# Kernel optimization log

Hardware: AMD Instinct MI355X
Metric: run time of the kernel (lower is better)

The kernel has to match this reference:

```python
import jax, jax.numpy as jnp
import numpy as np

NUM_GLOBAL_EXPERTS = 256
LOCAL_START = 64  # global experts [64, 128) live on this rank


def setup_inputs() -> dict:
    key = jax.random.key(0)
    k1, = jax.random.split(key, 1)
    num_local_experts = 64
    # Routing ids: ~4.2M tokens x topk=8, values are GLOBAL expert ids in [0, 256)
    topk_ids = jax.random.randint(k1, (33554432,), 0, NUM_GLOBAL_EXPERTS, dtype=jnp.int32)
    # expert_map: global -> local; -1 for experts not owned by this rank
    gid = jnp.arange(NUM_GLOBAL_EXPERTS, dtype=jnp.int32)
    expert_map = jnp.where(
        (gid >= LOCAL_START) & (gid < LOCAL_START + num_local_experts),
        gid - LOCAL_START,
        jnp.int32(-1),
    )
    return {"topk_ids": topk_ids, "num_local_experts": num_local_experts, "expert_map": expert_map}


def reference(topk_ids, num_local_experts, expert_map=None):
    n = num_local_experts  # static python int
    ids = topk_ids.reshape(-1)
    if expert_map is not None:
        # invalid ids (< 0) stay invalid; valid global ids are remapped to local space
        ids = jnp.where(ids >= 0, expert_map[jnp.clip(ids, 0)], jnp.int32(-1))
    # Route all invalid / out-of-range ids into an overflow bucket n, then drop it.
    valid = (ids >= 0) & (ids < n)
    bucket = jnp.where(valid, ids, jnp.int32(n))
    counts = jax.ops.segment_sum(
        jnp.ones_like(bucket, dtype=jnp.int32), bucket, num_segments=n + 1
    )
    return counts[:n].astype(jnp.int32)
```

## Files before the change

kernel.cpp:

```cpp
#include <hip/hip_runtime.h>

#define BLOCK   256
#define NB1     2048
#define NBINS   256
#define NWAVES  (BLOCK / 64)
#define UNROLL  4

__global__ __launch_bounds__(BLOCK) void hist_part(const int* __restrict__ ids,
                                                   int N,
                                                   int* __restrict__ partials) {
    __shared__ int lds[NWAVES * NBINS];
    const int tid = threadIdx.x;
    for (int i = tid; i < NWAVES * NBINS; i += BLOCK) lds[i] = 0;
    __syncthreads();

    int* h = &lds[(tid >> 6) * NBINS];

    const int4* __restrict__ ids4 = (const int4*)ids;
    const int n4      = N >> 2;
    const int chunk   = BLOCK * UNROLL;
    const int gstride = (int)gridDim.x * chunk;
    const int n4_full = (n4 / gstride) * gstride;

    for (int i = (int)blockIdx.x * chunk + tid; i < n4_full; i += gstride) {
        int4 v[UNROLL];
#pragma unroll
        for (int u = 0; u < UNROLL; ++u) v[u] = ids4[i + u * BLOCK];
#pragma unroll
        for (int u = 0; u < UNROLL; ++u) {
            atomicAdd(&h[v[u].x & (NBINS - 1)], 1);
            atomicAdd(&h[v[u].y & (NBINS - 1)], 1);
            atomicAdd(&h[v[u].z & (NBINS - 1)], 1);
            atomicAdd(&h[v[u].w & (NBINS - 1)], 1);
        }
    }
    for (int i = n4_full + (int)blockIdx.x * BLOCK + tid; i < n4;
         i += (int)gridDim.x * BLOCK) {
        int4 v = ids4[i];
        atomicAdd(&h[v.x & (NBINS - 1)], 1);
        atomicAdd(&h[v.y & (NBINS - 1)], 1);
        atomicAdd(&h[v.z & (NBINS - 1)], 1);
        atomicAdd(&h[v.w & (NBINS - 1)], 1);
    }
    if (blockIdx.x == 0) {
        for (int i = (n4 << 2) + tid; i < N; i += BLOCK)
            atomicAdd(&h[ids[i] & (NBINS - 1)], 1);
    }
    __syncthreads();

    for (int b = tid; b < NBINS; b += BLOCK) {
        int s = 0;
#pragma unroll
        for (int w = 0; w < NWAVES; ++w) s += lds[w * NBINS + b];
        partials[b * NB1 + blockIdx.x] = s;
    }
}

__global__ __launch_bounds__(BLOCK) void reduce_part(const int* __restrict__ partials,
                                                     const int* __restrict__ emap,
                                                     int emap_n,
                                                     int* __restrict__ out,
                                                     int n_local) {
    const int g = blockIdx.x;
    const int tid = threadIdx.x;
    int s = 0;
    for (int j = tid; j < NB1; j += BLOCK) s += partials[g * NB1 + j];
#pragma unroll
    for (int off = 32; off > 0; off >>= 1) s += __shfl_down(s, off, 64);
    __shared__ int wsum[NWAVES];
    if ((tid & 63) == 0) wsum[tid >> 6] = s;
    __syncthreads();
    if (tid == 0) {
        int tot = 0;
#pragma unroll
        for (int w = 0; w < NWAVES; ++w) tot += wsum[w];
        int l = (g < emap_n) ? emap[g] : -1;
        if ((unsigned)l < (unsigned)n_local && tot != 0) atomicAdd(&out[l], tot);
    }
}

extern "C" void kernel_launch(void* const* d_in, const int* in_sizes, int n_in,
                              void* d_out, int out_size, void* d_ws, size_t ws_size,
                              hipStream_t stream) {
    const int* topk_ids   = (const int*)d_in[0];
    const int* expert_map = (const int*)d_in[2];
    const int N       = in_sizes[0];
    const int emap_n  = in_sizes[2];
    const int n_local = out_size;

    int* partials = (int*)d_ws;

    hipMemsetAsync(d_out, 0, (size_t)n_local * sizeof(int), stream);

    hist_part<<<NB1, BLOCK, 0, stream>>>(topk_ids, N, partials);
    reduce_part<<<NBINS, BLOCK, 0, stream>>>(partials, expert_map, emap_n,
                                             (int*)d_out, n_local);
}
```

Baseline: 199.9 us.

## Remap expert ids inside histogram and skip non-local ids via affine map detection

Adds a prep kernel that checks whether expert_map is a contiguous affine range and records its base and count. The histogram kernel then either subtracts the base and bounds-checks, or looks each id up in an LDS copy of the map, so only local experts get atomics. This replaces the memset and the per-bin emap lookups in the reduce stage, and the reduce now runs over n_local bins only. The cost is an extra tiny kernel launch plus per-element compare and branch work, in exchange for roughly three quarters fewer LDS atomics.

```diff
diff --git a/kernel.cpp b/kernel.cpp
--- a/kernel.cpp
+++ b/kernel.cpp
@@ -6,15 +6,50 @@
 #define NWAVES  (BLOCK / 64)
 #define UNROLL  4
 
+#define PARTIALS_OFF 4096
+
+__global__ __launch_bounds__(BLOCK) void prep(const int* __restrict__ emap,
+                                              int emap_n,
+                                              int* __restrict__ params) {
+    __shared__ int s_min, s_cnt, s_ok;
+    const int tid = threadIdx.x;
+    if (tid == 0) { s_min = 0x7FFFFFFF; s_cnt = 0; s_ok = 1; }
+    __syncthreads();
+    for (int g = tid; g < emap_n; g += BLOCK) {
+        if (emap[g] >= 0) { atomicMin(&s_min, g); atomicAdd(&s_cnt, 1); }
+    }
+    __syncthreads();
+    const int lo = s_min, cnt = s_cnt;
+    for (int g = tid; g < emap_n; g += BLOCK) {
+        int expect = (g >= lo && g < lo + cnt) ? (g - lo) : -1;
+        if (emap[g] != expect) atomicAnd(&s_ok, 0);
+    }
+    __syncthreads();
+    if (tid == 0) { params[0] = lo; params[1] = cnt; params[2] = s_ok; }
+}
+
 __global__ __launch_bounds__(BLOCK) void hist_part(const int* __restrict__ ids,
                                                    int N,
-                                                   int* __restrict__ partials) {
-    __shared__ int lds[NWAVES * NBINS];
+                                                   const int* __restrict__ params,
+                                                   const int* __restrict__ emap,
+                                                   int emap_n,
+                                                   int* __restrict__ partials,
+                                                   int n_local) {
+    __shared__ int hist[NWAVES * NBINS];
+    __shared__ int lmap[NBINS];
     const int tid = threadIdx.x;
-    for (int i = tid; i < NWAVES * NBINS; i += BLOCK) lds[i] = 0;
+    const int lo = params[0];
+    const unsigned cnt = (unsigned)params[1];
+    const int affine = params[2];
+
+    for (int i = tid; i < NWAVES * NBINS; i += BLOCK) hist[i] = 0;
+    if (!affine) {
+        for (int i = tid; i < NBINS; i += BLOCK)
+            lmap[i] = (i < emap_n) ? emap[i] : -1;
+    }
     __syncthreads();
 
-    int* h = &lds[(tid >> 6) * NBINS];
+    int* h = &hist[(tid >> 6) * NBINS];
 
     const int4* __restrict__ ids4 = (const int4*)ids;
     const int n4      = N >> 2;
@@ -22,49 +57,92 @@
     const int gstride = (int)gridDim.x * chunk;
     const int n4_full = (n4 / gstride) * gstride;
 
-    for (int i = (int)blockIdx.x * chunk + tid; i < n4_full; i += gstride) {
-        int4 v[UNROLL];
+    if (affine) {
+        for (int i = (int)blockIdx.x * chunk + tid; i < n4_full; i += gstride) {
+            int4 v[UNROLL];
 #pragma unroll
-        for (int u = 0; u < UNROLL; ++u) v[u] = ids4[i + u * BLOCK];
+            for (int u = 0; u < UNROLL; ++u) v[u] = ids4[i + u * BLOCK];
 #pragma unroll
-        for (int u = 0; u < UNROLL; ++u) {
-            atomicAdd(&h[v[u].x & (NBINS - 1)], 1);
-            atomicAdd(&h[v[u].y & (NBINS - 1)], 1);
-            atomicAdd(&h[v[u].z & (NBINS - 1)], 1);
-            atomicAdd(&h[v[u].w & (NBINS - 1)], 1);
+            for (int u = 0; u < UNROLL; ++u) {
+                unsigned a = (unsigned)(v[u].x - lo);
+                unsigned b = (unsigned)(v[u].y - lo);
+                unsigned c = (unsigned)(v[u].z - lo);
+                unsigned d = (unsigned)(v[u].w - lo);
+                if (a < cnt) atomicAdd(&h[a], 1);
+                if (b < cnt) atomicAdd(&h[b], 1);
+                if (c < cnt) atomicAdd(&h[c], 1);
+                if (d < cnt) atomicAdd(&h[d], 1);
+            }
         }
-    }
-    for (int i = n4_full + (int)blockIdx.x * BLOCK + tid; i < n4;
-         i += (int)gridDim.x * BLOCK) {
-        int4 v = ids4[i];
-        atomicAdd(&h[v.x & (NBINS - 1)], 1);
-        atomicAdd(&h[v.y & (NBINS - 1)], 1);
-        atomicAdd(&h[v.z & (NBINS - 1)], 1);
-        atomicAdd(&h[v.w & (NBINS - 1)], 1);
-    }
-    if (blockIdx.x == 0) {
-        for (int i = (n4 << 2) + tid; i < N; i += BLOCK)
-            atomicAdd(&h[ids[i] & (NBINS - 1)], 1);
+        for (int i = n4_full + (int)blockIdx.x * BLOCK + tid; i < n4;
+             i += (int)gridDim.x * BLOCK) {
+            int4 v = ids4[i];
+            unsigned a = (unsigned)(v.x - lo), b = (unsigned)(v.y - lo);
+            unsigned c = (unsigned)(v.z - lo), d = (unsigned)(v.w - lo);
+            if (a < cnt) atomicAdd(&h[a], 1);
+            if (b < cnt) atomicAdd(&h[b], 1);
+            if (c < cnt) atomicAdd(&h[c], 1);
+            if (d < cnt) atomicAdd(&h[d], 1);
+        }
+        if (blockIdx.x == 0) {
+            for (int i = (n4 << 2) + tid; i < N; i += BLOCK) {
+                unsigned a = (unsigned)(ids[i] - lo);
+                if (a < cnt) atomicAdd(&h[a], 1);
+            }
+        }
+    } else {
+        for (int i = (int)blockIdx.x * chunk + tid; i < n4_full; i += gstride) {
+            int4 v[UNROLL];
+#pragma unroll
+            for (int u = 0; u < UNROLL; ++u) v[u] = ids4[i + u * BLOCK];
+#pragma unroll
+            for (int u = 0; u < UNROLL; ++u) {
+                int l0 = ((unsigned)v[u].x < NBINS) ? lmap[v[u].x] : -1;
+                int l1 = ((unsigned)v[u].y < NBINS) ? lmap[v[u].y] : -1;
+                int l2 = ((unsigned)v[u].z < NBINS) ? lmap[v[u].z] : -1;
+                int l3 = ((unsigned)v[u].w < NBINS) ? lmap[v[u].w] : -1;
+                if (l0 >= 0) atomicAdd(&h[l0], 1);
+                if (l1 >= 0) atomicAdd(&h[l1], 1);
+                if (l2 >= 0) atomicAdd(&h[l2], 1);
+                if (l3 >= 0) atomicAdd(&h[l3], 1);
+            }
+        }
+        for (int i = n4_full + (int)blockIdx.x * BLOCK + tid; i < n4;
+             i += (int)gridDim.x * BLOCK) {
+            int4 v = ids4[i];
+            int l0 = ((unsigned)v.x < NBINS) ? lmap[v.x] : -1;
+            int l1 = ((unsigned)v.y < NBINS) ? lmap[v.y] : -1;
+            int l2 = ((unsigned)v.z < NBINS) ? lmap[v.z] : -1;
+            int l3 = ((unsigned)v.w < NBINS) ? lmap[v.w] : -1;
+            if (l0 >= 0) atomicAdd(&h[l0], 1);
+            if (l1 >= 0) atomicAdd(&h[l1], 1);
+            if (l2 >= 0) atomicAdd(&h[l2], 1);
+            if (l3 >= 0) atomicAdd(&h[l3], 1);
+        }
+        if (blockIdx.x == 0) {
+            for (int i = (n4 << 2) + tid; i < N; i += BLOCK) {
+                int v = ids[i];
+                int l = ((unsigned)v < NBINS) ? lmap[v] : -1;
+                if (l >= 0) atomicAdd(&h[l], 1);
+            }
+        }
     }
     __syncthreads();
 
-    for (int b = tid; b < NBINS; b += BLOCK) {
+    for (int b = tid; b < n_local; b += BLOCK) {
         int s = 0;
 #pragma unroll
-        for (int w = 0; w < NWAVES; ++w) s += lds[w * NBINS + b];
+        for (int w = 0; w < NWAVES; ++w) s += hist[w * NBINS + b];
         partials[b * NB1 + blockIdx.x] = s;
     }
 }
 
 __global__ __launch_bounds__(BLOCK) void reduce_part(const int* __restrict__ partials,
-                                                     const int* __restrict__ emap,
-                                                     int emap_n,
-                                                     int* __restrict__ out,
-                                                     int n_local) {
-    const int g = blockIdx.x;
+                                                     int* __restrict__ out) {
+    const int b = blockIdx.x;
     const int tid = threadIdx.x;
     int s = 0;
-    for (int j = tid; j < NB1; j += BLOCK) s += partials[g * NB1 + j];
+    for (int j = tid; j < NB1; j += BLOCK) s += partials[b * NB1 + j];
 #pragma unroll
     for (int off = 32; off > 0; off >>= 1) s += __shfl_down(s, off, 64);
     __shared__ int wsum[NWAVES];
@@ -74,8 +152,7 @@
         int tot = 0;
 #pragma unroll
         for (int w = 0; w < NWAVES; ++w) tot += wsum[w];
-        int l = (g < emap_n) ? emap[g] : -1;
-        if ((unsigned)l < (unsigned)n_local && tot != 0) atomicAdd(&out[l], tot);
+        out[b] = tot;
     }
 }
 
@@ -88,11 +165,11 @@
     const int emap_n  = in_sizes[2];
     const int n_local = out_size;
 
-    int* partials = (int*)d_ws;
+    int* params   = (int*)d_ws;
+    int* partials = (int*)((char*)d_ws + PARTIALS_OFF);
 
-    hipMemsetAsync(d_out, 0, (size_t)n_local * sizeof(int), stream);
-
-    hist_part<<<NB1, BLOCK, 0, stream>>>(topk_ids, N, partials);
-    reduce_part<<<NBINS, BLOCK, 0, stream>>>(partials, expert_map, emap_n,
-                                             (int*)d_out, n_local);
+    prep<<<1, BLOCK, 0, stream>>>(expert_map, emap_n, params);
+    hist_part<<<NB1, BLOCK, 0, stream>>>(topk_ids, N, params, expert_map,
+                                         emap_n, partials, n_local);
+    reduce_part<<<n_local, BLOCK, 0, stream>>>(partials, (int*)d_out);
 }
```

New measurement: 196.4 us. No clear change (-1.7%).
